# Performance work log

Hardware: AMD Instinct MI355X
Metric: run time of the kernel (lower is better)

## Reference

```python
import jax, jax.numpy as jnp
import numpy as np

N = 50000
E = 800000
IN_C = 128
OUT_C = 256
NUM_REL = 6


def _rgcn_conv(x, src, dst, etype, W, root, bias):
    # PyG RGCNConv (no bases, aggr='mean'):
    # out = x @ root + bias + sum_r mean_{j in N_r(i)}(x_j) @ W[r]
    n = x.shape[0]
    xe = x[src]  # [E, d_in] gather of source features
    out = x @ root + bias
    for r in range(NUM_REL):
        m = (etype == r)
        s = jax.ops.segment_sum(jnp.where(m[:, None], xe, 0.0), dst, num_segments=n)
        c = jax.ops.segment_sum(m.astype(x.dtype), dst, num_segments=n)
        out = out + (s / jnp.maximum(c, 1.0)[:, None]) @ W[r]
    return out


def setup_inputs() -> dict:
    key = jax.random.key(0)
    ks = jax.random.split(key, 16)
    half = OUT_C // 2

    def g(k, shape, fan_in):
        return jax.random.normal(k, shape, dtype=jnp.float32) / np.sqrt(fan_in)

    return {
        "x": jax.random.normal(ks[0], (N, IN_C), dtype=jnp.float32),
        "edge_index": jax.random.randint(ks[1], (2, E), 0, N, dtype=jnp.int32),
        "edge_type": jax.random.randint(ks[2], (E,), 0, NUM_REL, dtype=jnp.int32),
        # encoder MLP
        "enc_w0": g(ks[3], (IN_C, OUT_C), IN_C), "enc_b0": jnp.zeros((OUT_C,), jnp.float32),
        "enc_w1": g(ks[4], (OUT_C, OUT_C), OUT_C), "enc_b1": jnp.zeros((OUT_C,), jnp.float32),
        "enc_w2": g(ks[5], (OUT_C, half), OUT_C), "enc_b2": jnp.zeros((half,), jnp.float32),
        # conv1
        "W1": g(ks[6], (NUM_REL, IN_C, OUT_C), IN_C), "root1": g(ks[7], (IN_C, OUT_C), IN_C),
        "b1": jnp.zeros((OUT_C,), jnp.float32),
        # conv2
        "W2": g(ks[8], (NUM_REL, OUT_C, OUT_C), OUT_C), "root2": g(ks[9], (OUT_C, OUT_C), OUT_C),
        "b2": jnp.zeros((OUT_C,), jnp.float32),
        # conv_out
        "W3": g(ks[10], (NUM_REL, OUT_C, half), OUT_C), "root3": g(ks[11], (OUT_C, half), OUT_C),
        "b3": jnp.zeros((half,), jnp.float32),
    }


def reference(x, edge_index, edge_type,
              enc_w0, enc_b0, enc_w1, enc_b1, enc_w2, enc_b2,
              W1, root1, b1, W2, root2, b2, W3, root3, b3):
    src, dst = edge_index[0], edge_index[1]
    # dense encoder branch
    h = jax.nn.relu(x @ enc_w0 + enc_b0)
    h = jax.nn.relu(h @ enc_w1 + enc_b1)
    self_feat = h @ enc_w2 + enc_b2
    # RGCN branch
    g1 = jax.nn.relu(_rgcn_conv(x, src, dst, edge_type, W1, root1, b1))
    g2 = jax.nn.relu(_rgcn_conv(g1, src, dst, edge_type, W2, root2, b2))
    graph_feat = _rgcn_conv(g2, src, dst, edge_type, W3, root3, b3)
    return jnp.concatenate([self_feat, graph_feat], axis=-1)
```

## Files before the change

### kernel.cpp

```cpp
#include <hip/hip_runtime.h>

#define NN   50000
#define EE   800000
#define INC  128
#define OUTC 256
#define HALF 128
#define NREL 6
#define NCELL (NN * NREL)
#define NPAD 50048

typedef __attribute__((ext_vector_type(4))) short s16x4;
typedef __attribute__((ext_vector_type(8))) short bf16x8;
typedef __attribute__((ext_vector_type(4))) float f32x4;

__device__ __forceinline__ float b2f(short b) {
    unsigned u = ((unsigned)(unsigned short)b) << 16;
    return __uint_as_float(u);
}
__device__ __forceinline__ short f2b(float f) {
    unsigned u = __float_as_uint(f);
    unsigned r = (u + 0x7fffu + ((u >> 16) & 1u)) >> 16;
    return (short)r;
}

__device__ __forceinline__ void gload16(const void* g, void* l) {
    __builtin_amdgcn_global_load_lds(
        (const __attribute__((address_space(1))) void*)g,
        (__attribute__((address_space(3))) void*)l, 16, 0, 0);
}

__global__ __launch_bounds__(256) void count_k(const int* __restrict__ dst,
                                               const int* __restrict__ et,
                                               int* __restrict__ cnt) {
    int e = blockIdx.x * 256 + threadIdx.x;
    if (e < EE) atomicAdd(&cnt[dst[e] * NREL + et[e]], 1);
}

__global__ __launch_bounds__(256) void scanA_k(const int* __restrict__ cnt,
                                               int* __restrict__ off,
                                               int* __restrict__ bsum, int n) {
    __shared__ int sh[256];
    int t = threadIdx.x;
    int base = blockIdx.x * 512 + t * 2;
    int v0 = (base < n) ? cnt[base] : 0;
    int v1 = (base + 1 < n) ? cnt[base + 1] : 0;
    int s = v0 + v1;
    sh[t] = s; __syncthreads();
    for (int o = 1; o < 256; o <<= 1) {
        int u = (t >= o) ? sh[t - o] : 0;
        __syncthreads();
        sh[t] += u;
        __syncthreads();
    }
    int excl = sh[t] - s;
    if (base < n)     off[base]     = excl;
    if (base + 1 < n) off[base + 1] = excl + v0;
    if (t == 255) bsum[blockIdx.x] = sh[255];
}

__global__ __launch_bounds__(1024) void scanB_k(int* __restrict__ bsum, int nb) {
    __shared__ int sh[1024];
    int t = threadIdx.x;
    int s = (t < nb) ? bsum[t] : 0;
    sh[t] = s; __syncthreads();
    for (int o = 1; o < 1024; o <<= 1) {
        int u = (t >= o) ? sh[t - o] : 0;
        __syncthreads();
        sh[t] += u;
        __syncthreads();
    }
    if (t < nb) bsum[t] = sh[t] - s;
}

__global__ __launch_bounds__(256) void scanC_k(int* __restrict__ off,
                                               const int* __restrict__ bsum, int n) {
    int i = blockIdx.x * 256 + threadIdx.x;
    if (i < n) off[i] += bsum[i >> 9];
    if (i == 0) off[n] = EE;
}

__global__ __launch_bounds__(256) void copyint_k(const int* __restrict__ a,
                                                 int* __restrict__ b, int n) {
    int i = blockIdx.x * 256 + threadIdx.x;
    if (i < n) b[i] = a[i];
}

__global__ __launch_bounds__(256) void fill_k(const int* __restrict__ src,
                                              const int* __restrict__ dst,
                                              const int* __restrict__ et,
                                              int* __restrict__ cur,
                                              int* __restrict__ es) {
    int e = blockIdx.x * 256 + threadIdx.x;
    if (e < EE) {
        int key = dst[e] * NREL + et[e];
        int p = atomicAdd(&cur[key], 1);
        es[p] = src[e];
    }
}

__global__ __launch_bounds__(256) void wgt_k(const int* __restrict__ off,
                                             const int* __restrict__ es,
                                             int* __restrict__ ep,
                                             float* __restrict__ wgt) {
    int c = blockIdx.x * 256 + threadIdx.x;
    if (c >= NCELL) return;
    int beg = off[c], end = off[c + 1];
    if (end <= beg) return;
    float inv = 1.f / (float)(end - beg);
    int rtag = (c % NREL) << 24;
    for (int p = beg; p < end; ++p) {
        ep[p] = es[p] | rtag;
        wgt[p] = inv;
    }
}

__global__ __launch_bounds__(256) void cast_x_k(const float* __restrict__ x,
                                                short* __restrict__ xb, int n4) {
    int i = blockIdx.x * 256 + threadIdx.x;
    if (i < n4) {
        float4 v = ((const float4*)x)[i];
        s16x4 o;
        o[0] = f2b(v.x); o[1] = f2b(v.y); o[2] = f2b(v.z); o[3] = f2b(v.w);
        ((s16x4*)xb)[i] = o;
    }
}

__global__ __launch_bounds__(256) void wtcat2_k(const float* __restrict__ root,
                                                const float* __restrict__ W,
                                                int K, int D, int Ncols,
                                                short* __restrict__ BT) {
    int i = blockIdx.x * 256 + threadIdx.x;
    if (i >= Ncols * K) return;
    int n = i / K, k = i - n * K;
    float v;
    if (n < D) {
        v = root[(size_t)k * D + n];
    } else {
        int nn = n - D;
        int r = nn / D, c = nn - r * D;
        v = W[((size_t)r * K + k) * D + c];
    }
    BT[(size_t)n * K + k] = f2b(v);
}

#define ACH(R, q) ((((R) << 2) | ((q) ^ ((R) & 3) ^ (((R) >> 2) & 1))) * 8)

__global__ __launch_bounds__(256) void gemm2_k(
    const short* __restrict__ A1, const short* __restrict__ B1,
    const float* __restrict__ bias1, int relu1,
    short* __restrict__ Cb1, int ldcb1, float* __restrict__ Cf1, int ldcf1,
    const short* __restrict__ A2, const short* __restrict__ B2,
    const float* __restrict__ bias2, int relu2,
    short* __restrict__ Cb2, int ldcb2, float* __restrict__ Cf2, int ldcf2,
    int M, int K, int nby1) {
    __shared__ __align__(16) char smem[16384];
    short* As = (short*)smem;
    short* Bs = As + 128 * 32;
    const int tid = threadIdx.x;
    const int wave = tid >> 6, lane = tid & 63;
    const int wm = (wave & 1) * 64, wn = (wave >> 1) * 64;
    const int l16 = lane & 15, quad = lane >> 4;
    const int bm = blockIdx.x * 128;

    const short* A; const short* BT; const float* bias;
    int relu; short* Cb; int ldcb; float* Cf; int ldcf; int bn;
    if ((int)blockIdx.y < nby1) {
        A = A1; BT = B1; bias = bias1; relu = relu1;
        Cb = Cb1; ldcb = ldcb1; Cf = Cf1; ldcf = ldcf1;
        bn = blockIdx.y * 128;
    } else {
        A = A2; BT = B2; bias = bias2; relu = relu2;
        Cb = Cb2; ldcb = ldcb2; Cf = Cf2; ldcf = ldcf2;
        bn = (blockIdx.y - nby1) * 128;
    }

    const int s0 = tid, s1 = tid + 256;
    const int r0 = s0 >> 2, c0 = (s0 & 3) ^ (r0 & 3) ^ ((r0 >> 2) & 1);
    const int r1 = s1 >> 2, c1 = (s1 & 3) ^ (r1 & 3) ^ ((r1 >> 2) & 1);

    f32x4 acc[4][4];
    #pragma unroll
    for (int i = 0; i < 4; ++i)
        #pragma unroll
        for (int j = 0; j < 4; ++j)
            acc[i][j] = (f32x4)0.f;

    for (int k0 = 0; k0 < K; k0 += 32) {
        gload16(A + (size_t)(bm + r0) * K + k0 + c0 * 8, As + s0 * 8);
        gload16(A + (size_t)(bm + r1) * K + k0 + c1 * 8, As + s1 * 8);
        gload16(BT + (size_t)(bn + r0) * K + k0 + c0 * 8, Bs + s0 * 8);
        gload16(BT + (size_t)(bn + r1) * K + k0 + c1 * 8, Bs + s1 * 8);
        __syncthreads();
        bf16x8 af[4], bf[4];
        #pragma unroll
        for (int mt = 0; mt < 4; ++mt)
            af[mt] = *(const bf16x8*)&As[ACH(wm + mt * 16 + l16, quad)];
        #pragma unroll
        for (int nt = 0; nt < 4; ++nt)
            bf[nt] = *(const bf16x8*)&Bs[ACH(wn + nt * 16 + l16, quad)];
        #pragma unroll
        for (int mt = 0; mt < 4; ++mt)
            #pragma unroll
            for (int nt = 0; nt < 4; ++nt)
                acc[mt][nt] = __builtin_amdgcn_mfma_f32_16x16x32_bf16(
                    af[mt], bf[nt], acc[mt][nt], 0, 0, 0);
        __syncthreads();
    }

    float bv[4];
    #pragma unroll
    for (int nt = 0; nt < 4; ++nt)
        bv[nt] = bias ? bias[bn + wn + nt * 16 + l16] : 0.f;

    if (Cb) {
        short* Es = (short*)smem;
        #pragma unroll
        for (int mt = 0; mt < 4; ++mt) {
            __syncthreads();
            int srb = (wave & 1) * 16 + quad * 4;
            #pragma unroll
            for (int nt = 0; nt < 4; ++nt) {
                int sc = wn + nt * 16 + l16;
                #pragma unroll
                for (int r = 0; r < 4; ++r) {
                    float v = acc[mt][nt][r] + bv[nt];
                    if (relu) v = fmaxf(v, 0.f);
                    Es[(srb + r) * 128 + sc] = f2b(v);
                }
            }
            __syncthreads();
            #pragma unroll
            for (int h = 0; h < 2; ++h) {
                int c = tid + h * 256;
                int rr = c >> 4, cc = c & 15;
                int grow = bm + (rr >> 4) * 64 + mt * 16 + (rr & 15);
                if (grow < M)
                    *(bf16x8*)(Cb + (size_t)grow * ldcb + bn + cc * 8) =
                        *(const bf16x8*)&Es[rr * 128 + cc * 8];
            }
        }
    } else {
        float* Ef = (float*)smem;
        #pragma unroll
        for (int mt = 0; mt < 4; ++mt) {
            __syncthreads();
            int srb = (wave & 1) * 16 + quad * 4;
            #pragma unroll
            for (int nt = 0; nt < 4; ++nt) {
                int sc = wn + nt * 16 + l16;
                #pragma unroll
                for (int r = 0; r < 4; ++r) {
                    float v = acc[mt][nt][r] + bv[nt];
                    if (relu) v = fmaxf(v, 0.f);
                    Ef[(srb + r) * 128 + sc] = v;
                }
            }
            __syncthreads();
            #pragma unroll
            for (int h = 0; h < 4; ++h) {
                int c = tid + h * 256;
                int rr = c >> 5, cc = c & 31;
                int grow = bm + (rr >> 4) * 64 + mt * 16 + (rr & 15);
                if (grow < M)
                    *(float4*)(Cf + (size_t)grow * ldcf + bn + cc * 4) =
                        *(const float4*)&Ef[rr * 128 + cc * 4];
            }
        }
    }
}

template<int D>
__global__ __launch_bounds__(256) void gagg2_k(
    const short* __restrict__ H, int ldh,
    const int* __restrict__ off,
    const int* __restrict__ ep, const float* __restrict__ wgt,
    const float* __restrict__ bias, int relu,
    short* __restrict__ Ob, float* __restrict__ Of, int ldo) {
    constexpr int LPN = D / 4;
    constexpr int NPB = 256 / LPN;
    int sub = threadIdx.x / LPN, lane = threadIdx.x % LPN;
    int node = blockIdx.x * NPB + sub;
    if (node >= NN) return;
    int c0 = lane * 4;
    const short* Hc = H + c0 + D;

    s16x4 sv = *(const s16x4*)(H + (size_t)node * ldh + c0);
    float a0 = b2f(sv[0]), a1 = b2f(sv[1]), a2 = b2f(sv[2]), a3 = b2f(sv[3]);

    int jb = off[node * NREL], je = off[node * NREL + NREL];
    int j = jb;
    for (; j + 3 < je; j += 4) {
        int u0 = ep[j], u1 = ep[j + 1], u2 = ep[j + 2], u3 = ep[j + 3];
        float w0 = wgt[j], w1 = wgt[j + 1], w2 = wgt[j + 2], w3 = wgt[j + 3];
        s16x4 x0 = *(const s16x4*)(Hc + (size_t)(u0 & 0xFFFFFF) * ldh + (u0 >> 24) * D);
        s16x4 x1 = *(const s16x4*)(Hc + (size_t)(u1 & 0xFFFFFF) * ldh + (u1 >> 24) * D);
        s16x4 x2 = *(const s16x4*)(Hc + (size_t)(u2 & 0xFFFFFF) * ldh + (u2 >> 24) * D);
        s16x4 x3 = *(const s16x4*)(Hc + (size_t)(u3 & 0xFFFFFF) * ldh + (u3 >> 24) * D);
        a0 += w0 * b2f(x0[0]) + w1 * b2f(x1[0]) + w2 * b2f(x2[0]) + w3 * b2f(x3[0]);
        a1 += w0 * b2f(x0[1]) + w1 * b2f(x1[1]) + w2 * b2f(x2[1]) + w3 * b2f(x3[1]);
        a2 += w0 * b2f(x0[2]) + w1 * b2f(x1[2]) + w2 * b2f(x2[2]) + w3 * b2f(x3[2]);
        a3 += w0 * b2f(x0[3]) + w1 * b2f(x1[3]) + w2 * b2f(x2[3]) + w3 * b2f(x3[3]);
    }
    for (; j < je; ++j) {
        int u = ep[j]; float w = wgt[j];
        s16x4 x = *(const s16x4*)(Hc + (size_t)(u & 0xFFFFFF) * ldh + (u >> 24) * D);
        a0 += w * b2f(x[0]); a1 += w * b2f(x[1]);
        a2 += w * b2f(x[2]); a3 += w * b2f(x[3]);
    }
    if (bias) {
        float4 bv = *(const float4*)(bias + c0);
        a0 += bv.x; a1 += bv.y; a2 += bv.z; a3 += bv.w;
    }
    if (relu) {
        a0 = fmaxf(a0, 0.f); a1 = fmaxf(a1, 0.f);
        a2 = fmaxf(a2, 0.f); a3 = fmaxf(a3, 0.f);
    }
    if (Ob) {
        s16x4 o;
        o[0] = f2b(a0); o[1] = f2b(a1); o[2] = f2b(a2); o[3] = f2b(a3);
        *(s16x4*)(Ob + (size_t)node * ldo + c0) = o;
    } else {
        float4 o; o.x = a0; o.y = a1; o.z = a2; o.w = a3;
        *(float4*)(Of + (size_t)node * ldo + c0) = o;
    }
}

template<int D>
__global__ __launch_bounds__(256) void gagg_k(
    const short* __restrict__ H, int ldh,
    int rfirst, int rlast, int colbase, int self0,
    const int* __restrict__ off, const int* __restrict__ es,
    const float* __restrict__ accin,
    const float* __restrict__ bias, int relu,
    short* __restrict__ Ob, float* __restrict__ Of, int ldo) {
    constexpr int LPN = D / 4;
    constexpr int NPB = 256 / LPN;
    int sub = threadIdx.x / LPN, lane = threadIdx.x % LPN;
    int node = blockIdx.x * NPB + sub;
    if (node >= NN) return;
    int c0 = lane * 4;

    float a0, a1, a2, a3;
    if (accin) {
        float4 t = *(const float4*)(accin + (size_t)node * D + c0);
        a0 = t.x; a1 = t.y; a2 = t.z; a3 = t.w;
    } else {
        a0 = a1 = a2 = a3 = 0.f;
    }
    if (self0) {
        s16x4 v = *(const s16x4*)(H + (size_t)node * ldh + c0);
        a0 += b2f(v[0]); a1 += b2f(v[1]); a2 += b2f(v[2]); a3 += b2f(v[3]);
    }
    int cell0 = node * NREL;
    for (int r = rfirst; r < rlast; ++r) {
        int beg = off[cell0 + r], end = off[cell0 + r + 1];
        if (end == beg) continue;
        int colo = (colbase + r) * D + c0;
        float s0 = 0.f, s1 = 0.f, s2 = 0.f, s3 = 0.f;
        int j = beg;
        for (; j + 1 < end; j += 2) {
            s16x4 v = *(const s16x4*)(H + (size_t)es[j] * ldh + colo);
            s16x4 w = *(const s16x4*)(H + (size_t)es[j + 1] * ldh + colo);
            s0 += b2f(v[0]) + b2f(w[0]);
            s1 += b2f(v[1]) + b2f(w[1]);
            s2 += b2f(v[2]) + b2f(w[2]);
            s3 += b2f(v[3]) + b2f(w[3]);
        }
        if (j < end) {
            s16x4 v = *(const s16x4*)(H + (size_t)es[j] * ldh + colo);
            s0 += b2f(v[0]); s1 += b2f(v[1]); s2 += b2f(v[2]); s3 += b2f(v[3]);
        }
        float inv = 1.f / (float)(end - beg);
        a0 += s0 * inv; a1 += s1 * inv; a2 += s2 * inv; a3 += s3 * inv;
    }
    if (bias) {
        float4 bv = *(const float4*)(bias + c0);
        a0 += bv.x; a1 += bv.y; a2 += bv.z; a3 += bv.w;
    }
    if (relu) {
        a0 = fmaxf(a0, 0.f); a1 = fmaxf(a1, 0.f);
        a2 = fmaxf(a2, 0.f); a3 = fmaxf(a3, 0.f);
    }
    if (Ob) {
        s16x4 o;
        o[0] = f2b(a0); o[1] = f2b(a1); o[2] = f2b(a2); o[3] = f2b(a3);
        *(s16x4*)(Ob + (size_t)node * ldo + c0) = o;
    } else {
        float4 o; o.x = a0; o.y = a1; o.z = a2; o.w = a3;
        *(float4*)(Of + (size_t)node * ldo + c0) = o;
    }
}

extern "C" void kernel_launch(void* const* d_in, const int* in_sizes, int n_in,
                              void* d_out, int out_size, void* d_ws, size_t ws_size,
                              hipStream_t stream) {
    const float* x      = (const float*)d_in[0];
    const int*   ei     = (const int*)d_in[1];
    const int*   srcv   = ei;
    const int*   dstv   = ei + EE;
    const int*   et     = (const int*)d_in[2];
    const float* enc_w0 = (const float*)d_in[3];
    const float* enc_b0 = (const float*)d_in[4];
    const float* enc_w1 = (const float*)d_in[5];
    const float* enc_b1 = (const float*)d_in[6];
    const float* enc_w2 = (const float*)d_in[7];
    const float* enc_b2 = (const float*)d_in[8];
    const float* W1     = (const float*)d_in[9];
    const float* root1  = (const float*)d_in[10];
    const float* b1     = (const float*)d_in[11];
    const float* W2     = (const float*)d_in[12];
    const float* root2  = (const float*)d_in[13];
    const float* b2     = (const float*)d_in[14];
    const float* W3     = (const float*)d_in[15];
    const float* root3  = (const float*)d_in[16];
    const float* b3     = (const float*)d_in[17];
    float* out = (float*)d_out;

    char* p = (char*)d_ws;
    auto alloc = [&](size_t bytes) -> char* {
        char* r = p; p += (bytes + 255) & ~(size_t)255; return r;
    };
    short* xb  = (short*)alloc((size_t)NPAD * INC * 2);
    short* g1  = (short*)alloc((size_t)NPAD * OUTC * 2);
    short* g2  = (short*)alloc((size_t)NPAD * OUTC * 2);
    short* BT1 = (short*)alloc((size_t)1792 * INC * 2);
    short* BT2 = (short*)alloc((size_t)1792 * OUTC * 2);
    short* BT3 = (short*)alloc((size_t)896 * OUTC * 2);
    short* ET0 = (short*)alloc((size_t)OUTC * INC * 2);
    short* ET1 = (short*)alloc((size_t)OUTC * OUTC * 2);
    short* ET2 = (short*)alloc((size_t)HALF * OUTC * 2);
    int* CNT  = (int*)alloc((size_t)NCELL * 4);
    int* OFF  = (int*)alloc((size_t)(NCELL + 1) * 4);
    int* CUR  = (int*)alloc((size_t)NCELL * 4);
    int* ES   = (int*)alloc((size_t)EE * 4);
    int* EP   = (int*)alloc((size_t)EE * 4);
    float* WG = (float*)alloc((size_t)EE * 4);
    int* BSUM = (int*)alloc(1024 * 4);
    size_t fixed = (size_t)(p - (char*)d_ws);

    const size_t Hfull = (size_t)NPAD * 1792 * 2;
    const size_t Esz   = (size_t)NPAD * OUTC * 2;
    bool tierA = fixed + Hfull + 2 * Esz + 1024 <= ws_size;
    bool fullH = tierA || (fixed + Hfull + 1024 <= ws_size);
    short* H = (short*)alloc(fullH ? Hfull : (size_t)NPAD * 1024 * 2);
    short* e1 = nullptr; short* e2 = nullptr; float* ACC = nullptr;
    if (tierA) { e1 = (short*)alloc(Esz); e2 = (short*)alloc(Esz); }
    if (!fullH) ACC = (float*)alloc((size_t)NPAD * OUTC * 4);

    hipMemsetAsync(CNT, 0, (size_t)NCELL * 4, stream);
    count_k<<<EE / 256, 256, 0, stream>>>(dstv, et, CNT);
    int nbA = (NCELL + 511) / 512;
    scanA_k<<<nbA, 256, 0, stream>>>(CNT, OFF, BSUM, NCELL);
    scanB_k<<<1, 1024, 0, stream>>>(BSUM, nbA);
    scanC_k<<<(NCELL + 255) / 256, 256, 0, stream>>>(OFF, BSUM, NCELL);
    copyint_k<<<(NCELL + 255) / 256, 256, 0, stream>>>(OFF, CUR, NCELL);
    fill_k<<<EE / 256, 256, 0, stream>>>(srcv, dstv, et, CUR, ES);
    wgt_k<<<(NCELL + 255) / 256, 256, 0, stream>>>(OFF, ES, EP, WG);

    cast_x_k<<<(NN * INC / 4 + 255) / 256, 256, 0, stream>>>(x, xb, NN * INC / 4);
    auto wt = [&](const float* root, const float* W, int K, int D, int Ncols, short* BT) {
        wtcat2_k<<<(Ncols * K + 255) / 256, 256, 0, stream>>>(root, W, K, D, Ncols, BT);
    };
    wt(root1, W1, INC, OUTC, 1792, BT1);
    wt(root2, W2, OUTC, OUTC, 1792, BT2);
    wt(root3, W3, OUTC, HALF, 896, BT3);
    wt(enc_w0, nullptr, INC, OUTC, OUTC, ET0);
    wt(enc_w1, nullptr, OUTC, OUTC, OUTC, ET1);
    wt(enc_w2, nullptr, OUTC, HALF, HALF, ET2);

    auto gemm1 = [&](const short* A, const short* BT, int M, int K, int Ncols,
                     const float* bias, int relu, short* Cb, int ldcb, float* Cf, int ldcf) {
        dim3 grid((M + 127) / 128, Ncols / 128);
        gemm2_k<<<grid, 256, 0, stream>>>(A, BT, bias, relu, Cb, ldcb, Cf, ldcf,
                                          A, BT, bias, relu, Cb, ldcb, Cf, ldcf,
                                          M, K, grid.y);
    };

    if (tierA) {
        gemm2_k<<<dim3(391, 16), 256, 0, stream>>>(
            xb, BT1, nullptr, 0, H, 1792, nullptr, 0,
            xb, ET0, enc_b0, 1, e1, OUTC, nullptr, 0,
            NN, INC, 14);
        gagg2_k<256><<<12500, 256, 0, stream>>>(H, 1792, OFF, EP, WG,
            b1, 1, g1, nullptr, OUTC);
        gemm2_k<<<dim3(391, 16), 256, 0, stream>>>(
            g1, BT2, nullptr, 0, H, 1792, nullptr, 0,
            e1, ET1, enc_b1, 1, e2, OUTC, nullptr, 0,
            NN, OUTC, 14);
        gagg2_k<256><<<12500, 256, 0, stream>>>(H, 1792, OFF, EP, WG,
            b2, 1, g2, nullptr, OUTC);
        gemm2_k<<<dim3(391, 8), 256, 0, stream>>>(
            g2, BT3, nullptr, 0, H, 896, nullptr, 0,
            e2, ET2, enc_b2, 0, nullptr, 0, out, OUTC,
            NN, OUTC, 7);
        gagg2_k<128><<<6250, 256, 0, stream>>>(H, 896, OFF, EP, WG,
            b3, 0, nullptr, out + HALF, OUTC);
        return;
    }

    gemm1(xb, ET0, NN, INC, OUTC, enc_b0, 1, g1, OUTC, nullptr, 0);
    gemm1(g1, ET1, NN, OUTC, OUTC, enc_b1, 1, g2, OUTC, nullptr, 0);
    gemm1(g2, ET2, NN, OUTC, HALF, enc_b2, 0, nullptr, 0, out, OUTC);

    auto conv = [&](const short* A, int K, int D, const short* BT,
                    const float* bias, int relu, short* Ob, float* Of) {
        int NPB = 256 / (D / 4);
        int gg = (NN + NPB - 1) / NPB;
        if (fullH) {
            gemm1(A, BT, NN, K, 7 * D, nullptr, 0, H, 7 * D, nullptr, 0);
            if (D == 256)
                gagg_k<256><<<gg, 256, 0, stream>>>(H, 7 * D, 0, NREL, 1, 1,
                    OFF, ES, nullptr, bias, relu, Ob, Of, OUTC);
            else
                gagg_k<128><<<gg, 256, 0, stream>>>(H, 7 * D, 0, NREL, 1, 1,
                    OFF, ES, nullptr, bias, relu, Ob, Of, OUTC);
        } else {
            gemm1(A, BT, NN, K, 4 * D, nullptr, 0, H, 4 * D, nullptr, 0);
            if (D == 256)
                gagg_k<256><<<gg, 256, 0, stream>>>(H, 4 * D, 0, 3, 1, 1,
                    OFF, ES, nullptr, nullptr, 0, nullptr, ACC, D);
            else
                gagg_k<128><<<gg, 256, 0, stream>>>(H, 4 * D, 0, 3, 1, 1,
                    OFF, ES, nullptr, nullptr, 0, nullptr, ACC, D);
            gemm1(A, BT + (size_t)4 * D * (size_t)K, NN, K, 3 * D, nullptr, 0, H, 3 * D, nullptr, 0);
            if (D == 256)
                gagg_k<256><<<gg, 256, 0, stream>>>(H, 3 * D, 3, NREL, -3, 0,
                    OFF, ES, ACC, bias, relu, Ob, Of, OUTC);
            else
                gagg_k<128><<<gg, 256, 0, stream>>>(H, 3 * D, 3, NREL, -3, 0,
                    OFF, ES, ACC, bias, relu, Ob, Of, OUTC);
        }
    };

    conv(xb, INC,  OUTC, BT1, b1, 1, g1, nullptr);
    conv(g1, OUTC, OUTC, BT2, b2, 1, g2, nullptr);
    conv(g2, OUTC, HALF, BT3, b3, 0, nullptr, out + HALF);
}
```

Measured before the change: 736.2 us.

## Assign one wavefront per node in gather-aggregate, splitting edges across lane groups

The edge-aggregation kernel now gives each node a full 64-lane wavefront. Lanes are split into groups that each process different edges in parallel with 8-wide bf16 loads, and the partial sums are combined by a cross-lane shuffle reduction. The aim is more memory-level parallelism per node and wider loads, instead of one short serial edge loop per node. The cost is shuffle-reduction overhead and idle lanes for low-degree nodes; the D=128 launch grid is doubled to match four nodes per block.

Result: no change. 736.9 us (+0.1%).

```diff
diff --git a/kernel.cpp b/kernel.cpp
--- a/kernel.cpp
+++ b/kernel.cpp
@@ -276,52 +276,65 @@
     const int* __restrict__ ep, const float* __restrict__ wgt,
     const float* __restrict__ bias, int relu,
     short* __restrict__ Ob, float* __restrict__ Of, int ldo) {
-    constexpr int LPN = D / 4;
-    constexpr int NPB = 256 / LPN;
-    int sub = threadIdx.x / LPN, lane = threadIdx.x % LPN;
-    int node = blockIdx.x * NPB + sub;
+    constexpr int LPR = D / 8;
+    constexpr int RPW = 64 / LPR;
+    constexpr int U   = 4;
+    int wave = threadIdx.x >> 6, lane = threadIdx.x & 63;
+    int node = blockIdx.x * 4 + wave;
     if (node >= NN) return;
-    int c0 = lane * 4;
-    const short* Hc = H + c0 + D;
-
-    s16x4 sv = *(const s16x4*)(H + (size_t)node * ldh + c0);
-    float a0 = b2f(sv[0]), a1 = b2f(sv[1]), a2 = b2f(sv[2]), a3 = b2f(sv[3]);
+    int er = lane / LPR, cl = lane % LPR;
+    int c0 = cl * 8;
+    const short* Hc = H + D + c0;
+
+    float a[8];
+    #pragma unroll
+    for (int k = 0; k < 8; ++k) a[k] = 0.f;
 
     int jb = off[node * NREL], je = off[node * NREL + NREL];
-    int j = jb;
-    for (; j + 3 < je; j += 4) {
-        int u0 = ep[j], u1 = ep[j + 1], u2 = ep[j + 2], u3 = ep[j + 3];
-        float w0 = wgt[j], w1 = wgt[j + 1], w2 = wgt[j + 2], w3 = wgt[j + 3];
-        s16x4 x0 = *(const s16x4*)(Hc + (size_t)(u0 & 0xFFFFFF) * ldh + (u0 >> 24) * D);
-        s16x4 x1 = *(const s16x4*)(Hc + (size_t)(u1 & 0xFFFFFF) * ldh + (u1 >> 24) * D);
-        s16x4 x2 = *(const s16x4*)(Hc + (size_t)(u2 & 0xFFFFFF) * ldh + (u2 >> 24) * D);
-        s16x4 x3 = *(const s16x4*)(Hc + (size_t)(u3 & 0xFFFFFF) * ldh + (u3 >> 24) * D);
-        a0 += w0 * b2f(x0[0]) + w1 * b2f(x1[0]) + w2 * b2f(x2[0]) + w3 * b2f(x3[0]);
-        a1 += w0 * b2f(x0[1]) + w1 * b2f(x1[1]) + w2 * b2f(x2[1]) + w3 * b2f(x3[1]);
-        a2 += w0 * b2f(x0[2]) + w1 * b2f(x1[2]) + w2 * b2f(x2[2]) + w3 * b2f(x3[2]);
-        a3 += w0 * b2f(x0[3]) + w1 * b2f(x1[3]) + w2 * b2f(x2[3]) + w3 * b2f(x3[3]);
-    }
-    for (; j < je; ++j) {
-        int u = ep[j]; float w = wgt[j];
-        s16x4 x = *(const s16x4*)(Hc + (size_t)(u & 0xFFFFFF) * ldh + (u >> 24) * D);
-        a0 += w * b2f(x[0]); a1 += w * b2f(x[1]);
-        a2 += w * b2f(x[2]); a3 += w * b2f(x[3]);
-    }
-    if (bias) {
-        float4 bv = *(const float4*)(bias + c0);
-        a0 += bv.x; a1 += bv.y; a2 += bv.z; a3 += bv.w;
-    }
-    if (relu) {
-        a0 = fmaxf(a0, 0.f); a1 = fmaxf(a1, 0.f);
-        a2 = fmaxf(a2, 0.f); a3 = fmaxf(a3, 0.f);
-    }
-    if (Ob) {
-        s16x4 o;
-        o[0] = f2b(a0); o[1] = f2b(a1); o[2] = f2b(a2); o[3] = f2b(a3);
-        *(s16x4*)(Ob + (size_t)node * ldo + c0) = o;
-    } else {
-        float4 o; o.x = a0; o.y = a1; o.z = a2; o.w = a3;
-        *(float4*)(Of + (size_t)node * ldo + c0) = o;
+    for (int j = jb; j < je; j += RPW * U) {
+        #pragma unroll
+        for (int u = 0; u < U; ++u) {
+            int idx = j + u * RPW + er;
+            bool v = idx < je;
+            int uu = v ? ep[idx] : 0;
+            float w = v ? wgt[idx] : 0.f;
+            bf16x8 x = *(const bf16x8*)(Hc + (size_t)(uu & 0xFFFFFF) * ldh
+                                           + (uu >> 24) * D);
+            #pragma unroll
+            for (int k = 0; k < 8; ++k) a[k] += w * b2f(x[k]);
+        }
+    }
+
+    #pragma unroll
+    for (int s = LPR; s < 64; s <<= 1)
+        #pragma unroll
+        for (int k = 0; k < 8; ++k)
+            a[k] += __shfl_xor(a[k], s, 64);
+
+    if (er == 0) {
+        bf16x8 sv = *(const bf16x8*)(H + (size_t)node * ldh + c0);
+        #pragma unroll
+        for (int k = 0; k < 8; ++k) a[k] += b2f(sv[k]);
+        if (bias) {
+            #pragma unroll
+            for (int k = 0; k < 8; ++k) a[k] += bias[c0 + k];
+        }
+        if (relu) {
+            #pragma unroll
+            for (int k = 0; k < 8; ++k) a[k] = fmaxf(a[k], 0.f);
+        }
+        if (Ob) {
+            bf16x8 o;
+            #pragma unroll
+            for (int k = 0; k < 8; ++k) o[k] = f2b(a[k]);
+            *(bf16x8*)(Ob + (size_t)node * ldo + c0) = o;
+        } else {
+            f32x4 o0, o1;
+            #pragma unroll
+            for (int k = 0; k < 4; ++k) { o0[k] = a[k]; o1[k] = a[k + 4]; }
+            *(f32x4*)(Of + (size_t)node * ldo + c0) = o0;
+            *(f32x4*)(Of + (size_t)node * ldo + c0 + 4) = o1;
+        }
     }
 }
 
@@ -493,7 +506,7 @@
             g2, BT3, nullptr, 0, H, 896, nullptr, 0,
             e2, ET2, enc_b2, 0, nullptr, 0, out, OUTC,
             NN, OUTC, 7);
-        gagg2_k<128><<<6250, 256, 0, stream>>>(H, 896, OFF, EP, WG,
+        gagg2_k<128><<<12500, 256, 0, stream>>>(H, 896, OFF, EP, WG,
             b3, 0, nullptr, out + HALF, OUTC);
         return;
     }
```
